# Kernel optimization log

Hardware: AMD Instinct MI355X
Metric: run time of the kernel (lower is better)

The kernel has to match this reference:

```python
import jax, jax.numpy as jnp
import numpy as np

N = 300000      # number of documents
F = 136         # LTR features (MSLR-style)
H1, H2 = 128, 64
NPAIRS = 23     # ceil(sqrt(random_pairs=500))
SIGMA = 1.0


def setup_inputs() -> dict:
    key = jax.random.key(0)
    ks = jax.random.split(key, 9)
    x = jax.random.normal(ks[0], (N, F), dtype=jnp.float32)
    W1 = jax.random.normal(ks[1], (F, H1), dtype=jnp.float32) * 0.08
    b1 = jnp.zeros((H1,), jnp.float32)
    W2 = jax.random.normal(ks[2], (H1, H2), dtype=jnp.float32) * 0.08
    b2 = jnp.zeros((H2,), jnp.float32)
    Wout = jax.random.normal(ks[3], (H2, 1), dtype=jnp.float32) * 0.08
    bout = jnp.zeros((1,), jnp.float32)
    target = jax.random.randint(ks[4], (N,), 0, 5).astype(jnp.float32)
    random_docs = jax.random.randint(ks[5], (NPAIRS,), 0, N, dtype=jnp.int32)
    return {"x": x, "W1": W1, "b1": b1, "W2": W2, "b2": b2,
            "Wout": Wout, "bout": bout, "target": target,
            "random_docs": random_docs}


def reference(x, W1, b1, W2, b2, Wout, bout, target, random_docs):
    # scoring network (dropout = eval-mode identity)
    h = jax.nn.relu(x @ W1 + b1)
    h = jax.nn.relu(h @ W2 + b2)
    scores = (h @ Wout + bout)[:, 0]              # [N]

    # LambdaRank pseudo-loss over sampled docs (faithful incl. original bugs)
    t = jax.lax.stop_gradient(target)             # labels are detached in torch code
    labels = t[random_docs]                       # [n]
    n = labels.shape[0]
    w = 1.0 / jnp.arange(1, n + 1, dtype=jnp.float32)   # ERR rank weights 1/r
    # ERR(swap(x,y)) - ERR(orig) = (labels[y]-labels[x]) * (w[x]-w[y])
    absD = jnp.abs((labels[None, :] - labels[:, None]) * (w[:, None] - w[None, :]))  # [n,n]
    # z_j = s_i bug => calc_p == 0.5 always => lambda_ij = sigma*(0.5*(1-S) - 0.5)
    S = jnp.sign(labels[:, None] - labels[None, :])
    lam = SIGMA * (0.5 * (1.0 - S) - 0.5)
    # skip when sampled doc indices are equal (i == j on doc ids, not positions)
    mask = (random_docs[:, None] != random_docs[None, :]).astype(jnp.float32)
    # lambda_i / delta_i never reset across outer loop -> running cumulative sums
    cumL = jnp.cumsum(jnp.sum(lam * mask, axis=1))
    cumD = jnp.cumsum(jnp.sum(absD * mask, axis=1))
    s = scores[random_docs]                       # [n]
    loss = jnp.sum(cumL * cumD * s)
    return loss.reshape(1)
```

## Files before the change

### kernel.cpp

```cpp
#include <hip/hip_runtime.h>

#define NDOCS 23
#define FDIM 136
#define H1DIM 128
#define H2DIM 64
#define SIGMA 1.0f
#define NTHREADS 1024
#define G1 8
#define F_PER_G 17
#define G2 16
#define I_PER_G 8
#define XT_PITCH 24
#define H1T_PITCH 24
#define H2_PITCH 68

__global__ __launch_bounds__(NTHREADS) void lambdarank_loss_kernel(
    const float* __restrict__ x,
    const float* __restrict__ W1,
    const float* __restrict__ b1,
    const float* __restrict__ W2,
    const float* __restrict__ b2,
    const float* __restrict__ Wout,
    const float* __restrict__ bout,
    const float* __restrict__ target,
    const int*   __restrict__ docs,
    float* __restrict__ out)
{
    __shared__ float s_part[G1 * NDOCS * H1DIM];
    __shared__ float s_xT[FDIM * XT_PITCH];
    __shared__ float s_h1T[H1DIM * H1T_PITCH];
    __shared__ float s_h2[NDOCS * H2_PITCH];
    __shared__ int   s_docs[NDOCS];
    __shared__ float s_labels[NDOCS];
    __shared__ float s_score[NDOCS];
    __shared__ float s_rowL[NDOCS];
    __shared__ float s_rowD[NDOCS];

    const int tid = threadIdx.x;

    if (tid < NDOCS) {
        int d = docs[tid];
        s_docs[tid] = d;
        s_labels[tid] = target[d];
    }
    __syncthreads();

    for (int idx = tid; idx < NDOCS * FDIM; idx += NTHREADS) {
        int k = idx / FDIM;
        int f = idx - k * FDIM;
        s_xT[f * XT_PITCH + k] = x[(long long)s_docs[k] * FDIM + f];
    }
    __syncthreads();

    {
        const int j = tid & (H1DIM - 1);
        const int g = tid >> 7;
        float acc[NDOCS];
        #pragma unroll
        for (int k = 0; k < NDOCS; ++k) acc[k] = 0.0f;
        const int f0 = g * F_PER_G;
        #pragma unroll
        for (int ff = 0; ff < F_PER_G; ++ff) {
            const int f = f0 + ff;
            const float w = W1[f * H1DIM + j];
            alignas(16) float xv[XT_PITCH];
            #pragma unroll
            for (int q = 0; q < XT_PITCH / 4; ++q)
                *reinterpret_cast<float4*>(&xv[q * 4]) =
                    *reinterpret_cast<const float4*>(&s_xT[f * XT_PITCH + q * 4]);
            #pragma unroll
            for (int k = 0; k < NDOCS; ++k)
                acc[k] = fmaf(xv[k], w, acc[k]);
        }
        #pragma unroll
        for (int k = 0; k < NDOCS; ++k)
            s_part[(g * NDOCS + k) * H1DIM + j] = acc[k];
    }
    __syncthreads();

    for (int idx = tid; idx < NDOCS * H1DIM; idx += NTHREADS) {
        int k = idx >> 7;
        int j = idx & (H1DIM - 1);
        float a = b1[j];
        #pragma unroll
        for (int g = 0; g < G1; ++g)
            a += s_part[(g * NDOCS + k) * H1DIM + j];
        s_h1T[j * H1T_PITCH + k] = fmaxf(a, 0.0f);
    }
    __syncthreads();

    {
        const int j = tid & (H2DIM - 1);
        const int g = tid >> 6;
        float acc[NDOCS];
        #pragma unroll
        for (int k = 0; k < NDOCS; ++k) acc[k] = 0.0f;
        const int i0 = g * I_PER_G;
        #pragma unroll
        for (int ii = 0; ii < I_PER_G; ++ii) {
            const int i = i0 + ii;
            const float w = W2[i * H2DIM + j];
            alignas(16) float hv[H1T_PITCH];
            #pragma unroll
            for (int q = 0; q < H1T_PITCH / 4; ++q)
                *reinterpret_cast<float4*>(&hv[q * 4]) =
                    *reinterpret_cast<const float4*>(&s_h1T[i * H1T_PITCH + q * 4]);
            #pragma unroll
            for (int k = 0; k < NDOCS; ++k)
                acc[k] = fmaf(hv[k], w, acc[k]);
        }
        #pragma unroll
        for (int k = 0; k < NDOCS; ++k)
            s_part[(g * NDOCS + k) * H2DIM + j] = acc[k];
    }
    __syncthreads();

    for (int idx = tid; idx < NDOCS * H2DIM; idx += NTHREADS) {
        int k = idx >> 6;
        int j = idx & (H2DIM - 1);
        float a = b2[j];
        #pragma unroll
        for (int g = 0; g < G2; ++g)
            a += s_part[(g * NDOCS + k) * H2DIM + j];
        s_h2[k * H2_PITCH + j] = fmaxf(a, 0.0f);
    }
    __syncthreads();

    if (tid < NDOCS) {
        float acc = bout[0];
        #pragma unroll 8
        for (int i = 0; i < H2DIM; ++i)
            acc = fmaf(s_h2[tid * H2_PITCH + i], Wout[i], acc);
        s_score[tid] = acc;

        const float li = s_labels[tid];
        const float wi = 1.0f / (float)(tid + 1);
        const int   di = s_docs[tid];
        float rl = 0.0f, rd = 0.0f;
        for (int j = 0; j < NDOCS; ++j) {
            if (s_docs[j] == di) continue;
            const float lj = s_labels[j];
            const float wj = 1.0f / (float)(j + 1);
            const float dl = li - lj;
            const float S  = (dl > 0.0f) ? 1.0f : ((dl < 0.0f) ? -1.0f : 0.0f);
            rl += SIGMA * (0.5f * (1.0f - S) - 0.5f);
            rd += fabsf((lj - li) * (wi - wj));
        }
        s_rowL[tid] = rl;
        s_rowD[tid] = rd;
    }
    __syncthreads();

    if (tid == 0) {
        float cl = 0.0f, cd = 0.0f, loss = 0.0f;
        for (int i = 0; i < NDOCS; ++i) {
            cl += s_rowL[i];
            cd += s_rowD[i];
            loss += cl * cd * s_score[i];
        }
        out[0] = loss;
    }
}

extern "C" void kernel_launch(void* const* d_in, const int* in_sizes, int n_in,
                              void* d_out, int out_size, void* d_ws, size_t ws_size,
                              hipStream_t stream) {
    const float* x      = (const float*)d_in[0];
    const float* W1     = (const float*)d_in[1];
    const float* b1     = (const float*)d_in[2];
    const float* W2     = (const float*)d_in[3];
    const float* b2     = (const float*)d_in[4];
    const float* Wout   = (const float*)d_in[5];
    const float* bout   = (const float*)d_in[6];
    const float* target = (const float*)d_in[7];
    const int*   docs   = (const int*)d_in[8];
    float* out = (float*)d_out;

    hipLaunchKernelGGL(lambdarank_loss_kernel, dim3(1), dim3(NTHREADS), 0, stream,
                       x, W1, b1, W2, b2, Wout, bout, target, docs, out);
}
```

Baseline: 17.65 us.

## Prefetch weights into registers, vectorize gather, fuse output layer via wave shuffles

New measurement: 17.29 us. 1.02x faster.

```diff
diff --git a/kernel.cpp b/kernel.cpp
--- a/kernel.cpp
+++ b/kernel.cpp
@@ -12,7 +12,6 @@
 #define I_PER_G 8
 #define XT_PITCH 24
 #define H1T_PITCH 24
-#define H2_PITCH 68
 
 __global__ __launch_bounds__(NTHREADS) void lambdarank_loss_kernel(
     const float* __restrict__ x,
@@ -29,7 +28,6 @@
     __shared__ float s_part[G1 * NDOCS * H1DIM];
     __shared__ float s_xT[FDIM * XT_PITCH];
     __shared__ float s_h1T[H1DIM * H1T_PITCH];
-    __shared__ float s_h2[NDOCS * H2_PITCH];
     __shared__ int   s_docs[NDOCS];
     __shared__ float s_labels[NDOCS];
     __shared__ float s_score[NDOCS];
@@ -38,31 +36,53 @@
 
     const int tid = threadIdx.x;
 
-    if (tid < NDOCS) {
-        int d = docs[tid];
-        s_docs[tid] = d;
-        s_labels[tid] = target[d];
-    }
-    __syncthreads();
-
-    for (int idx = tid; idx < NDOCS * FDIM; idx += NTHREADS) {
-        int k = idx / FDIM;
-        int f = idx - k * FDIM;
-        s_xT[f * XT_PITCH + k] = x[(long long)s_docs[k] * FDIM + f];
-    }
+    int dd = 0;
+    if (tid < 64) dd = docs[tid < NDOCS ? tid : 0];
+
+    const int j1 = tid & (H1DIM - 1);
+    const int g1 = tid >> 7;
+    float w1r[F_PER_G];
+    #pragma unroll
+    for (int ff = 0; ff < F_PER_G; ++ff)
+        w1r[ff] = W1[(g1 * F_PER_G + ff) * H1DIM + j1];
+
+    const int j2 = tid & (H2DIM - 1);
+    const int g2 = tid >> 6;
+    float w2r[I_PER_G];
+    #pragma unroll
+    for (int ii = 0; ii < I_PER_G; ++ii)
+        w2r[ii] = W2[(g2 * I_PER_G + ii) * H2DIM + j2];
+
+    const float b1r   = b1[j1];
+    const float b2r   = b2[j2];
+    const float woutr = Wout[j2];
+    const float boutr = bout[0];
+
+    if (tid < NDOCS) s_docs[tid] = dd;
+    __syncthreads();
+
+    float lb = 0.0f;
+    if (tid < 64) lb = target[dd];
+    if (tid < NDOCS * (FDIM / 4)) {
+        const int q = tid / NDOCS;
+        const int k = tid - q * NDOCS;
+        const float4 v = *reinterpret_cast<const float4*>(
+            &x[(long long)s_docs[k] * FDIM + q * 4]);
+        s_xT[(q * 4 + 0) * XT_PITCH + k] = v.x;
+        s_xT[(q * 4 + 1) * XT_PITCH + k] = v.y;
+        s_xT[(q * 4 + 2) * XT_PITCH + k] = v.z;
+        s_xT[(q * 4 + 3) * XT_PITCH + k] = v.w;
+    }
+    if (tid < NDOCS) s_labels[tid] = lb;
     __syncthreads();
 
     {
-        const int j = tid & (H1DIM - 1);
-        const int g = tid >> 7;
         float acc[NDOCS];
         #pragma unroll
         for (int k = 0; k < NDOCS; ++k) acc[k] = 0.0f;
-        const int f0 = g * F_PER_G;
         #pragma unroll
         for (int ff = 0; ff < F_PER_G; ++ff) {
-            const int f = f0 + ff;
-            const float w = W1[f * H1DIM + j];
+            const int f = g1 * F_PER_G + ff;
             alignas(16) float xv[XT_PITCH];
             #pragma unroll
             for (int q = 0; q < XT_PITCH / 4; ++q)
@@ -70,36 +90,36 @@
                     *reinterpret_cast<const float4*>(&s_xT[f * XT_PITCH + q * 4]);
             #pragma unroll
             for (int k = 0; k < NDOCS; ++k)
-                acc[k] = fmaf(xv[k], w, acc[k]);
+                acc[k] = fmaf(xv[k], w1r[ff], acc[k]);
         }
         #pragma unroll
         for (int k = 0; k < NDOCS; ++k)
-            s_part[(g * NDOCS + k) * H1DIM + j] = acc[k];
-    }
-    __syncthreads();
-
-    for (int idx = tid; idx < NDOCS * H1DIM; idx += NTHREADS) {
-        int k = idx >> 7;
-        int j = idx & (H1DIM - 1);
-        float a = b1[j];
-        #pragma unroll
-        for (int g = 0; g < G1; ++g)
-            a += s_part[(g * NDOCS + k) * H1DIM + j];
-        s_h1T[j * H1T_PITCH + k] = fmaxf(a, 0.0f);
+            s_part[(g1 * NDOCS + k) * H1DIM + j1] = acc[k];
+    }
+    __syncthreads();
+
+    #pragma unroll
+    for (int m = 0; m < 3; ++m) {
+        const int idx = tid + m * NTHREADS;
+        if (idx < NDOCS * H1DIM) {
+            const int k = idx >> 7;
+            const int j = idx & (H1DIM - 1);
+            float a = b1r;
+            #pragma unroll
+            for (int g = 0; g < G1; ++g)
+                a += s_part[(g * NDOCS + k) * H1DIM + j];
+            s_h1T[j * H1T_PITCH + k] = fmaxf(a, 0.0f);
+        }
     }
     __syncthreads();
 
     {
-        const int j = tid & (H2DIM - 1);
-        const int g = tid >> 6;
         float acc[NDOCS];
         #pragma unroll
         for (int k = 0; k < NDOCS; ++k) acc[k] = 0.0f;
-        const int i0 = g * I_PER_G;
         #pragma unroll
         for (int ii = 0; ii < I_PER_G; ++ii) {
-            const int i = i0 + ii;
-            const float w = W2[i * H2DIM + j];
+            const int i = g2 * I_PER_G + ii;
             alignas(16) float hv[H1T_PITCH];
             #pragma unroll
             for (int q = 0; q < H1T_PITCH / 4; ++q)
@@ -107,35 +127,39 @@
                     *reinterpret_cast<const float4*>(&s_h1T[i * H1T_PITCH + q * 4]);
             #pragma unroll
             for (int k = 0; k < NDOCS; ++k)
-                acc[k] = fmaf(hv[k], w, acc[k]);
+                acc[k] = fmaf(hv[k], w2r[ii], acc[k]);
         }
         #pragma unroll
         for (int k = 0; k < NDOCS; ++k)
-            s_part[(g * NDOCS + k) * H2DIM + j] = acc[k];
-    }
-    __syncthreads();
-
-    for (int idx = tid; idx < NDOCS * H2DIM; idx += NTHREADS) {
-        int k = idx >> 6;
-        int j = idx & (H2DIM - 1);
-        float a = b2[j];
-        #pragma unroll
-        for (int g = 0; g < G2; ++g)
-            a += s_part[(g * NDOCS + k) * H2DIM + j];
-        s_h2[k * H2_PITCH + j] = fmaxf(a, 0.0f);
-    }
-    __syncthreads();
-
-    if (tid < NDOCS) {
-        float acc = bout[0];
-        #pragma unroll 8
-        for (int i = 0; i < H2DIM; ++i)
-            acc = fmaf(s_h2[tid * H2_PITCH + i], Wout[i], acc);
-        s_score[tid] = acc;
-
-        const float li = s_labels[tid];
-        const float wi = 1.0f / (float)(tid + 1);
-        const int   di = s_docs[tid];
+            s_part[(g2 * NDOCS + k) * H2DIM + j2] = acc[k];
+    }
+    __syncthreads();
+
+    #pragma unroll
+    for (int m = 0; m < 2; ++m) {
+        const int idx = tid + m * NTHREADS;
+        float c = 0.0f;
+        if (idx < NDOCS * H2DIM) {
+            const int k = idx >> 6;
+            const int i = idx & (H2DIM - 1);
+            float a = b2r;
+            #pragma unroll
+            for (int g = 0; g < G2; ++g)
+                a += s_part[(g * NDOCS + k) * H2DIM + i];
+            c = fmaxf(a, 0.0f) * woutr;
+        }
+        #pragma unroll
+        for (int off = 32; off > 0; off >>= 1)
+            c += __shfl_down(c, off, 64);
+        if ((tid & 63) == 0 && idx < NDOCS * H2DIM)
+            s_score[idx >> 6] = c + boutr;
+    }
+
+    if (tid >= 512 && tid < 512 + NDOCS) {
+        const int i  = tid - 512;
+        const float li = s_labels[i];
+        const float wi = 1.0f / (float)(i + 1);
+        const int   di = s_docs[i];
         float rl = 0.0f, rd = 0.0f;
         for (int j = 0; j < NDOCS; ++j) {
             if (s_docs[j] == di) continue;
@@ -146,8 +170,8 @@
             rl += SIGMA * (0.5f * (1.0f - S) - 0.5f);
             rd += fabsf((lj - li) * (wi - wj));
         }
-        s_rowL[tid] = rl;
-        s_rowD[tid] = rd;
+        s_rowL[i] = rl;
+        s_rowD[i] = rd;
     }
     __syncthreads();
 
```
